# Kernel tuning notes

Measured on AMD Instinct MI355X. Metric: run time of the kernel, lower is better.

The kernel has to match this reference:

```python
import jax, jax.numpy as jnp
import numpy as np

HEADS = 12
WINDOW = 128

def setup_inputs() -> dict:
    key = jax.random.key(0)
    ks = jax.random.split(key, 5)
    B, N, C = 1, 4096, 768
    return {
        'x': jax.random.normal(ks[0], (B, N, C), dtype=jnp.float32),
        'qkv_w': jax.random.normal(ks[1], (3 * C, C), dtype=jnp.float32) * 0.02,
        'qkv_b': jax.random.normal(ks[2], (3 * C,), dtype=jnp.float32) * 0.02,
        'proj_w': jax.random.normal(ks[3], (C, C), dtype=jnp.float32) * 0.02,
        'proj_b': jax.random.normal(ks[4], (C,), dtype=jnp.float32) * 0.02,
    }

def reference(x, qkv_w, qkv_b, proj_w, proj_b):
    B, N, C = x.shape
    H = HEADS
    hd = C // H
    # qkv projection (torch Linear: y = x @ W^T + b)
    qkv = x @ qkv_w.T + qkv_b                      # [B, N, 3C]
    qkv = qkv.reshape(B, N, 3, H, hd).transpose(2, 0, 3, 1, 4)  # [3, B, H, N, hd]
    q, k, v = qkv[0], qkv[1], qkv[2]               # each [B, H, N, hd]
    # local (banded) mask: |i - j| <= window_size
    idxs = jnp.arange(N)
    local = jnp.abs(idxs[:, None] - idxs[None, :]) <= WINDOW  # [N, N] bool
    # dense scores then mask (faithful to original O(N^2) math)
    attn = jnp.einsum('bhnd,bhmd->bhnm', q, k) / jnp.sqrt(jnp.float32(hd))
    attn = jnp.where(local[None, None], attn, -jnp.inf)
    attn = jax.nn.softmax(attn, axis=-1)
    out = jnp.einsum('bhnm,bhmd->bhnd', attn, v)   # [B, H, N, hd]
    out = out.transpose(0, 2, 1, 3).reshape(B, N, C)
    return out @ proj_w.T + proj_b
```

## Files before the change

### kernel.cpp

```cpp
#include <hip/hip_runtime.h>
#include <hip/hip_fp16.h>
#include <cmath>

typedef _Float16 f16;
typedef __attribute__((ext_vector_type(8))) _Float16 f16x8;
typedef __attribute__((ext_vector_type(4))) _Float16 f16x4;
typedef __attribute__((ext_vector_type(4))) float f32x4;

#define EXP2F(x) __builtin_amdgcn_exp2f(x)


__global__ void pack3_f32_f16(
    const float* __restrict__ s0, f16* __restrict__ d0, int nc0, int kc0,
    const float* __restrict__ s1, f16* __restrict__ d1, int nc1, int kc1,
    const float* __restrict__ s2, f16* __restrict__ d2, int nc2, int kc2)
{
    int wid  = (blockIdx.x * blockDim.x + threadIdx.x) >> 6;
    int lane = threadIdx.x & 63;
    const float* s; f16* d; int cid, KC;
    if (wid < nc0)                  { s = s0; d = d0; cid = wid;             KC = kc0; }
    else if (wid < nc0 + nc1)       { s = s1; d = d1; cid = wid - nc0;       KC = kc1; }
    else if (wid < nc0 + nc1 + nc2) { s = s2; d = d2; cid = wid - nc0 - nc1; KC = kc2; }
    else return;
    int rc = cid / KC, kc = cid % KC;
    int K  = KC << 5;
    const float* src = s + (size_t)(rc * 16 + (lane & 15)) * K + kc * 32 + (lane >> 4) * 8;
    float4 v0 = *(const float4*)src;
    float4 v1 = *(const float4*)(src + 4);
    f16x8 o = { (f16)v0.x, (f16)v0.y, (f16)v0.z, (f16)v0.w,
                (f16)v1.x, (f16)v1.y, (f16)v1.z, (f16)v1.w };
    *(f16x8*)(d + (size_t)cid * 512 + lane * 8) = o;
}

__device__ __forceinline__ void store4(f16* p, const f32x4& v) {
    f16x4 o = { (f16)v[0], (f16)v[1], (f16)v[2], (f16)v[3] };
    *(f16x4*)p = o;
}
__device__ __forceinline__ void store4(float* p, const f32x4& v) {
    float4 o = { v[0], v[1], v[2], v[3] };
    *(float4*)p = o;
}

template <int WR, int WC, int MT, int NT, typename OT>
__global__ __launch_bounds__(256) void gemm_f16_packed(
    const f16* __restrict__ Ap,
    const f16* __restrict__ Wp,
    const float* __restrict__ bias,
    OT* __restrict__ out,
    int M, int N, int K)
{
    constexpr int KK  = 2;
    constexpr int ACH = WR * MT * KK;
    constexpr int BCH = WC * NT * KK;
    constexpr int AR  = ACH / 4;
    constexpr int BR  = BCH / 4;
    __shared__ f16 Ash[2][ACH * 512];
    __shared__ f16 Bsh[2][BCH * 512];

    const int tid  = threadIdx.x;
    const int lane = tid & 63;
    const int w    = tid >> 6;
    const int wr   = w / WC;
    const int wc   = w % WC;
    const int lr   = lane & 15;
    const int lq   = lane >> 4;
    const int bm   = blockIdx.y * (WR * MT * 16);
    const int bn   = blockIdx.x * (WC * NT * 16);
    const int KC   = K >> 5;

    const f16* ga[AR];
    const f16* gb[BR];
#pragma unroll
    for (int r = 0; r < AR; ++r) {
        int s = w * AR + r, rl = s / KK, kk = s % KK;
        ga[r] = Ap + ((size_t)((bm >> 4) + rl) * KC + kk) * 512 + lane * 8;
    }
#pragma unroll
    for (int r = 0; r < BR; ++r) {
        int s = w * BR + r, rl = s / KK, kk = s % KK;
        gb[r] = Wp + ((size_t)((bn >> 4) + rl) * KC + kk) * 512 + lane * 8;
    }

    f32x4 acc[MT][NT] = {};
    f16x8 sa[AR], sb[BR];

#pragma unroll
    for (int r = 0; r < AR; ++r) sa[r] = *(const f16x8*)(ga[r]);
#pragma unroll
    for (int r = 0; r < BR; ++r) sb[r] = *(const f16x8*)(gb[r]);
#pragma unroll
    for (int r = 0; r < AR; ++r) *(f16x8*)&Ash[0][(w * AR + r) * 512 + lane * 8] = sa[r];
#pragma unroll
    for (int r = 0; r < BR; ++r) *(f16x8*)&Bsh[0][(w * BR + r) * 512 + lane * 8] = sb[r];
    __syncthreads();

    const int nk = K >> 6;
    for (int k = 0; k < nk; ++k) {
        const int cur = k & 1;
        if (k + 1 < nk) {
            const int ko = (k + 1) * KK * 512;
#pragma unroll
            for (int r = 0; r < AR; ++r) sa[r] = *(const f16x8*)(ga[r] + ko);
#pragma unroll
            for (int r = 0; r < BR; ++r) sb[r] = *(const f16x8*)(gb[r] + ko);
        }
        f16x8 af[MT][KK], bf[NT][KK];
#pragma unroll
        for (int mt = 0; mt < MT; ++mt)
#pragma unroll
            for (int kk = 0; kk < KK; ++kk)
                af[mt][kk] = *(const f16x8*)&Ash[cur][((wr * MT + mt) * KK + kk) * 512 + lane * 8];
#pragma unroll
        for (int nt = 0; nt < NT; ++nt)
#pragma unroll
            for (int kk = 0; kk < KK; ++kk)
                bf[nt][kk] = *(const f16x8*)&Bsh[cur][((wc * NT + nt) * KK + kk) * 512 + lane * 8];
#pragma unroll
        for (int kk = 0; kk < KK; ++kk)
#pragma unroll
            for (int mt = 0; mt < MT; ++mt)
#pragma unroll
                for (int nt = 0; nt < NT; ++nt)
                    acc[mt][nt] = __builtin_amdgcn_mfma_f32_16x16x32_f16(
                        bf[nt][kk], af[mt][kk], acc[mt][nt], 0, 0, 0);
        if (k + 1 < nk) {
#pragma unroll
            for (int r = 0; r < AR; ++r)
                *(f16x8*)&Ash[cur ^ 1][(w * AR + r) * 512 + lane * 8] = sa[r];
#pragma unroll
            for (int r = 0; r < BR; ++r)
                *(f16x8*)&Bsh[cur ^ 1][(w * BR + r) * 512 + lane * 8] = sb[r];
        }
        __syncthreads();
    }

#pragma unroll
    for (int mt = 0; mt < MT; ++mt) {
        int row = bm + (wr * MT + mt) * 16 + lr;
#pragma unroll
        for (int nt = 0; nt < NT; ++nt) {
            int col = bn + (wc * NT + nt) * 16 + lq * 4;
            float4 bv = *(const float4*)(bias + col);
            f32x4 ov = acc[mt][nt];
            ov[0] += bv.x; ov[1] += bv.y; ov[2] += bv.z; ov[3] += bv.w;
            store4(out + (size_t)row * N + col, ov);
        }
    }
}

#define WINDOW_SZ 128

__global__ __launch_bounds__(256) void local_attn_mfma(
    const f16* __restrict__ qkv,
    f16* __restrict__ outp,
    int N)
{
    const int C  = 768;
    const int C3 = 2304;
    __shared__ f16 Ks[2][4096];
    __shared__ f16 Vt[2][4096];
    __shared__ f16 Ps[4096];

    const int tid  = threadIdx.x;
    const int lane = tid & 63;
    const int w    = tid >> 6;
    const int r15  = lane & 15;
    const int q4   = lane >> 4;
    const int ntiles = N >> 6;
    const int h  = blockIdx.x / ntiles;
    const int i0 = (blockIdx.x % ntiles) << 6;
    const int qoff = h * 64;
    const int koff = 768 + h * 64;
    const int voff = 1536 + h * 64;

    f16x8 qf[2];
    {
        const f16* qrow = qkv + (size_t)(i0 + w * 16 + r15) * C3 + qoff + q4 * 8;
        qf[0] = *(const f16x8*)(qrow);
        qf[1] = *(const f16x8*)(qrow + 32);
        const f16 qs = (f16)0.18033688f;
#pragma unroll
        for (int j = 0; j < 8; ++j) { qf[0][j] *= qs; qf[1][j] *= qs; }
    }

    const int vc0 = tid >> 3;
    const int vd0 = (tid & 7) * 8;
    const int va  = vd0 >> 3;

    f32x4 o[4] = {};
    float m_l = -1.0e30f, l_l = 0.f;

    const int lo = (i0 >= 128) ? 0 : ((128 - i0) >> 6);
    int hi = (N + 64 - i0) >> 6; if (hi > 4) hi = 4;

    f16x8 k0, k1, v0, v1;
    {
        int jbase = i0 - 128 + lo * 64;
        const f16* kr = qkv + (size_t)(jbase + w * 16 + r15) * C3 + koff + q4 * 8;
        k0 = *(const f16x8*)(kr);
        k1 = *(const f16x8*)(kr + 32);
        v0 = *(const f16x8*)(qkv + (size_t)(jbase + vc0) * C3 + voff + vd0);
        v1 = *(const f16x8*)(qkv + (size_t)(jbase + vc0 + 32) * C3 + voff + vd0);
        *(f16x8*)&Ks[0][(w * 2 + 0) * 512 + lane * 8] = k0;
        *(f16x8*)&Ks[0][(w * 2 + 1) * 512 + lane * 8] = k1;
        int cc0 = vc0 >> 3, c7 = vc0 & 7;
#pragma unroll
        for (int j = 0; j < 8; ++j) {
            Vt[0][(vd0 + j) * 64 + ((cc0 ^ va ^ j) & 7) * 8 + c7] = v0[j];
            Vt[0][(vd0 + j) * 64 + (((cc0 + 4) ^ va ^ j) & 7) * 8 + c7] = v1[j];
        }
    }
    __syncthreads();

    for (int ch = lo; ch <= hi; ++ch) {
        const int p = (ch - lo) & 1;
        const int jbase = i0 - 128 + ch * 64;
        const bool need_mask = (ch == 0) || (ch == 4);

        if (ch < hi) {
            int jn = jbase + 64;
            const f16* kr = qkv + (size_t)(jn + w * 16 + r15) * C3 + koff + q4 * 8;
            k0 = *(const f16x8*)(kr);
            k1 = *(const f16x8*)(kr + 32);
            v0 = *(const f16x8*)(qkv + (size_t)(jn + vc0) * C3 + voff + vd0);
            v1 = *(const f16x8*)(qkv + (size_t)(jn + vc0 + 32) * C3 + voff + vd0);
        }

        f32x4 s[4] = {};
#pragma unroll
        for (int ks = 0; ks < 2; ++ks)
#pragma unroll
            for (int nt = 0; nt < 4; ++nt) {
                f16x8 kf = *(const f16x8*)&Ks[p][(nt * 2 + ks) * 512 + lane * 8];
                s[nt] = __builtin_amdgcn_mfma_f32_16x16x32_f16(kf, qf[ks], s[nt], 0, 0, 0);
            }

        if (need_mask) {
            int qg = i0 + w * 16 + r15;
#pragma unroll
            for (int nt = 0; nt < 4; ++nt)
#pragma unroll
                for (int r = 0; r < 4; ++r) {
                    int dist = qg - (jbase + nt * 16 + q4 * 4 + r);
                    if (dist < 0) dist = -dist;
                    if (dist > WINDOW_SZ) s[nt][r] = -3.0e38f;
                }
        }

        float rmax = -3.0e38f;
#pragma unroll
        for (int nt = 0; nt < 4; ++nt)
#pragma unroll
            for (int r = 0; r < 4; ++r) rmax = fmaxf(rmax, s[nt][r]);
        rmax = fmaxf(rmax, __shfl_xor(rmax, 16));
        rmax = fmaxf(rmax, __shfl_xor(rmax, 32));
        float mn = fmaxf(m_l, rmax);
        float al = EXP2F(m_l - mn);
        m_l = mn;
        float rs = 0.f;
#pragma unroll
        for (int nt = 0; nt < 4; ++nt)
#pragma unroll
            for (int r = 0; r < 4; ++r) {
                float pv = EXP2F(s[nt][r] - mn);
                s[nt][r] = pv;
                rs += pv;
            }
        rs += __shfl_xor(rs, 16);
        rs += __shfl_xor(rs, 32);
        l_l = l_l * al + rs;
#pragma unroll
        for (int nd = 0; nd < 4; ++nd)
#pragma unroll
            for (int r = 0; r < 4; ++r) o[nd][r] *= al;

#pragma unroll
        for (int nt = 0; nt < 4; ++nt)
#pragma unroll
            for (int r = 0; r < 4; ++r) {
                int c  = nt * 16 + q4 * 4 + r;
                int cs = c >> 5;
                int c5 = c & 31;
                int ls = (c5 >> 3) * 16 + r15;
                int lss = ls ^ ((ls >> 3) & 7);
                Ps[(w * 2 + cs) * 512 + lss * 8 + (c5 & 7)] = (f16)s[nt][r];
            }

        int lssr = lane ^ ((lane >> 3) & 7);
#pragma unroll
        for (int cs = 0; cs < 2; ++cs) {
            f16x8 pf = *(const f16x8*)&Ps[(w * 2 + cs) * 512 + lssr * 8];
#pragma unroll
            for (int nd = 0; nd < 4; ++nd) {
                int d = nd * 16 + r15;
                int x = ((cs * 4 + q4) ^ (d >> 3) ^ d) & 7;
                f16x8 vf = *(const f16x8*)&Vt[p][d * 64 + x * 8];
                o[nd] = __builtin_amdgcn_mfma_f32_16x16x32_f16(vf, pf, o[nd], 0, 0, 0);
            }
        }

        if (ch < hi) {
            *(f16x8*)&Ks[p ^ 1][(w * 2 + 0) * 512 + lane * 8] = k0;
            *(f16x8*)&Ks[p ^ 1][(w * 2 + 1) * 512 + lane * 8] = k1;
            int cc0 = vc0 >> 3, c7 = vc0 & 7;
#pragma unroll
            for (int j = 0; j < 8; ++j) {
                Vt[p ^ 1][(vd0 + j) * 64 + ((cc0 ^ va ^ j) & 7) * 8 + c7] = v0[j];
                Vt[p ^ 1][(vd0 + j) * 64 + (((cc0 + 4) ^ va ^ j) & 7) * 8 + c7] = v1[j];
            }
        }
        __syncthreads();
    }

    float inv = 1.0f / l_l;
    const int KC2 = C >> 5;
    const int rc  = (i0 >> 4) + w;
#pragma unroll
    for (int nd = 0; nd < 4; ++nd) {
        int col = qoff + nd * 16 + q4 * 4;
        int kc  = col >> 5;
        int lp  = r15 + ((col >> 3) & 3) * 16;
        f16x4 ov = { (f16)(o[nd][0] * inv), (f16)(o[nd][1] * inv),
                     (f16)(o[nd][2] * inv), (f16)(o[nd][3] * inv) };
        *(f16x4*)(outp + ((size_t)rc * KC2 + kc) * 512 + lp * 8 + (col & 7)) = ov;
    }
}

extern "C" void kernel_launch(void* const* d_in, const int* in_sizes, int n_in,
                              void* d_out, int out_size, void* d_ws, size_t ws_size,
                              hipStream_t stream) {
    (void)n_in; (void)out_size; (void)ws_size;
    const float* x      = (const float*)d_in[0];
    const float* qkv_w  = (const float*)d_in[1];
    const float* qkv_b  = (const float*)d_in[2];
    const float* proj_w = (const float*)d_in[3];
    const float* proj_b = (const float*)d_in[4];
    float* outp = (float*)d_out;

    const int C    = in_sizes[2] / 3;
    const int Nseq = in_sizes[0] / C;
    const int C3   = 3 * C;
    const int KC   = C >> 5;

    char* ws = (char*)d_ws;
    f16* qkv_h = (f16*)ws;   ws += (size_t)Nseq * C3 * 2;
    f16* xp    = (f16*)ws;   ws += (size_t)Nseq * C * 2;
    f16* wqp   = (f16*)ws;   ws += (size_t)C3 * C * 2;
    f16* wpp   = (f16*)ws;
    f16* attn_p = xp;

    dim3 blk(256);
    {
        int nc0 = (Nseq / 16) * KC;
        int nc1 = (C3 / 16) * KC;
        int nc2 = (C / 16) * KC;
        int nwaves = nc0 + nc1 + nc2;
        pack3_f32_f16<<<dim3((nwaves + 3) / 4), blk, 0, stream>>>(
            x, xp, nc0, KC, qkv_w, wqp, nc1, KC, proj_w, wpp, nc2, KC);
    }
    gemm_f16_packed<2, 2, 4, 4, f16><<<dim3(C3 / 128, Nseq / 128), blk, 0, stream>>>(
        xp, wqp, qkv_b, qkv_h, Nseq, C3, C);
    local_attn_mfma<<<dim3((C / 64) * (Nseq / 64)), blk, 0, stream>>>(
        qkv_h, attn_p, Nseq);
    gemm_f16_packed<2, 2, 2, 2, float><<<dim3(C / 64, Nseq / 64), blk, 0, stream>>>(
        attn_p, wpp, proj_b, outp, Nseq, C, C);
}
```

Baseline: 133.3 us.

## Emit QKV in MFMA-fragment packed layout and read K/V directly from global

The QKV GEMM epilogue now writes Q and K per head in the MFMA operand fragment layout, and V transposed and packed, so the attention kernel can load operand fragments straight from global memory. The attention kernel drops its LDS double buffers for K and V, the register staging and the per-chunk __syncthreads, which removes LDS traffic and barrier stalls. In exchange, the GEMM epilogue does scattered scalar f16 stores for V. K/V reuse across the four waves of a block now depends on the cache rather than shared memory.

```diff
diff --git a/kernel.cpp b/kernel.cpp
--- a/kernel.cpp
+++ b/kernel.cpp
@@ -8,7 +8,6 @@
 typedef __attribute__((ext_vector_type(4))) float f32x4;
 
 #define EXP2F(x) __builtin_amdgcn_exp2f(x)
-
 
 __global__ void pack3_f32_f16(
     const float* __restrict__ s0, f16* __restrict__ d0, int nc0, int kc0,
@@ -41,7 +40,7 @@
     *(float4*)p = o;
 }
 
-template <int WR, int WC, int MT, int NT, typename OT>
+template <int WR, int WC, int MT, int NT, int MODE, typename OT>
 __global__ __launch_bounds__(256) void gemm_f16_packed(
     const f16* __restrict__ Ap,
     const f16* __restrict__ Wp,
@@ -143,7 +142,29 @@
             float4 bv = *(const float4*)(bias + col);
             f32x4 ov = acc[mt][nt];
             ov[0] += bv.x; ov[1] += bv.y; ov[2] += bv.z; ov[3] += bv.w;
-            store4(out + (size_t)row * N + col, ov);
+            if (MODE == 0) {
+                store4(out + (size_t)row * N + col, ov);
+            } else {
+                int tau = (col >= 1536) ? 2 : (col >= 768 ? 1 : 0);
+                int rm  = col - tau * 768;
+                int hh  = rm >> 6;
+                int d   = rm & 63;
+                f16* base = (f16*)out + ((size_t)tau * 12 + hh) * ((size_t)M * 64);
+                if (tau < 2) {
+                    size_t off = (size_t)(row >> 4) * 1024 + (d >> 5) * 512
+                               + (size_t)((row & 15) + ((d >> 3) & 3) * 16) * 8 + (d & 7);
+                    store4(base + off, ov);
+                } else {
+#pragma unroll
+                    for (int i = 0; i < 4; ++i) {
+                        int dd = d + i;
+                        size_t off = (size_t)(dd >> 4) * ((size_t)M * 16)
+                                   + (size_t)(row >> 5) * 512
+                                   + (size_t)((dd & 15) + ((row >> 3) & 3) * 16) * 8 + (row & 7);
+                        base[off] = (f16)ov[i];
+                    }
+                }
+            }
         }
     }
 }
@@ -151,14 +172,11 @@
 #define WINDOW_SZ 128
 
 __global__ __launch_bounds__(256) void local_attn_mfma(
-    const f16* __restrict__ qkv,
+    const f16* __restrict__ qkvp,
     f16* __restrict__ outp,
     int N)
 {
-    const int C  = 768;
-    const int C3 = 2304;
-    __shared__ f16 Ks[2][4096];
-    __shared__ f16 Vt[2][4096];
+    const int C = 768;
     __shared__ f16 Ps[4096];
 
     const int tid  = threadIdx.x;
@@ -169,23 +187,22 @@
     const int ntiles = N >> 6;
     const int h  = blockIdx.x / ntiles;
     const int i0 = (blockIdx.x % ntiles) << 6;
-    const int qoff = h * 64;
-    const int koff = 768 + h * 64;
-    const int voff = 1536 + h * 64;
+
+    const size_t hstride = (size_t)N * 64;
+    const f16* Qh = qkvp + (size_t)h * hstride;
+    const f16* Kh = qkvp + (size_t)(12 + h) * hstride;
+    const f16* Vh = qkvp + (size_t)(24 + h) * hstride;
+    const int dcStride = N * 16;
 
     f16x8 qf[2];
     {
-        const f16* qrow = qkv + (size_t)(i0 + w * 16 + r15) * C3 + qoff + q4 * 8;
-        qf[0] = *(const f16x8*)(qrow);
-        qf[1] = *(const f16x8*)(qrow + 32);
+        const f16* qp = Qh + (size_t)((i0 >> 4) + w) * 1024 + lane * 8;
+        qf[0] = *(const f16x8*)(qp);
+        qf[1] = *(const f16x8*)(qp + 512);
         const f16 qs = (f16)0.18033688f;
 #pragma unroll
         for (int j = 0; j < 8; ++j) { qf[0][j] *= qs; qf[1][j] *= qs; }
     }
-
-    const int vc0 = tid >> 3;
-    const int vd0 = (tid & 7) * 8;
-    const int va  = vd0 >> 3;
 
     f32x4 o[4] = {};
     float m_l = -1.0e30f, l_l = 0.f;
@@ -193,45 +210,19 @@
     const int lo = (i0 >= 128) ? 0 : ((128 - i0) >> 6);
     int hi = (N + 64 - i0) >> 6; if (hi > 4) hi = 4;
 
-    f16x8 k0, k1, v0, v1;
-    {
-        int jbase = i0 - 128 + lo * 64;
-        const f16* kr = qkv + (size_t)(jbase + w * 16 + r15) * C3 + koff + q4 * 8;
-        k0 = *(const f16x8*)(kr);
-        k1 = *(const f16x8*)(kr + 32);
-        v0 = *(const f16x8*)(qkv + (size_t)(jbase + vc0) * C3 + voff + vd0);
-        v1 = *(const f16x8*)(qkv + (size_t)(jbase + vc0 + 32) * C3 + voff + vd0);
-        *(f16x8*)&Ks[0][(w * 2 + 0) * 512 + lane * 8] = k0;
-        *(f16x8*)&Ks[0][(w * 2 + 1) * 512 + lane * 8] = k1;
-        int cc0 = vc0 >> 3, c7 = vc0 & 7;
-#pragma unroll
-        for (int j = 0; j < 8; ++j) {
-            Vt[0][(vd0 + j) * 64 + ((cc0 ^ va ^ j) & 7) * 8 + c7] = v0[j];
-            Vt[0][(vd0 + j) * 64 + (((cc0 + 4) ^ va ^ j) & 7) * 8 + c7] = v1[j];
-        }
-    }
-    __syncthreads();
+    const int lssr = lane ^ ((lane >> 3) & 7);
 
     for (int ch = lo; ch <= hi; ++ch) {
-        const int p = (ch - lo) & 1;
         const int jbase = i0 - 128 + ch * 64;
         const bool need_mask = (ch == 0) || (ch == 4);
 
-        if (ch < hi) {
-            int jn = jbase + 64;
-            const f16* kr = qkv + (size_t)(jn + w * 16 + r15) * C3 + koff + q4 * 8;
-            k0 = *(const f16x8*)(kr);
-            k1 = *(const f16x8*)(kr + 32);
-            v0 = *(const f16x8*)(qkv + (size_t)(jn + vc0) * C3 + voff + vd0);
-            v1 = *(const f16x8*)(qkv + (size_t)(jn + vc0 + 32) * C3 + voff + vd0);
-        }
-
         f32x4 s[4] = {};
 #pragma unroll
         for (int ks = 0; ks < 2; ++ks)
 #pragma unroll
             for (int nt = 0; nt < 4; ++nt) {
-                f16x8 kf = *(const f16x8*)&Ks[p][(nt * 2 + ks) * 512 + lane * 8];
+                f16x8 kf = *(const f16x8*)(Kh + (size_t)((jbase >> 4) + nt) * 1024
+                                              + ks * 512 + lane * 8);
                 s[nt] = __builtin_amdgcn_mfma_f32_16x16x32_f16(kf, qf[ks], s[nt], 0, 0, 0);
             }
 
@@ -286,30 +277,16 @@
                 Ps[(w * 2 + cs) * 512 + lss * 8 + (c5 & 7)] = (f16)s[nt][r];
             }
 
-        int lssr = lane ^ ((lane >> 3) & 7);
 #pragma unroll
         for (int cs = 0; cs < 2; ++cs) {
             f16x8 pf = *(const f16x8*)&Ps[(w * 2 + cs) * 512 + lssr * 8];
 #pragma unroll
             for (int nd = 0; nd < 4; ++nd) {
-                int d = nd * 16 + r15;
-                int x = ((cs * 4 + q4) ^ (d >> 3) ^ d) & 7;
-                f16x8 vf = *(const f16x8*)&Vt[p][d * 64 + x * 8];
+                f16x8 vf = *(const f16x8*)(Vh + (size_t)nd * dcStride
+                                              + (size_t)((jbase >> 5) + cs) * 512 + lane * 8);
                 o[nd] = __builtin_amdgcn_mfma_f32_16x16x32_f16(vf, pf, o[nd], 0, 0, 0);
             }
         }
-
-        if (ch < hi) {
-            *(f16x8*)&Ks[p ^ 1][(w * 2 + 0) * 512 + lane * 8] = k0;
-            *(f16x8*)&Ks[p ^ 1][(w * 2 + 1) * 512 + lane * 8] = k1;
-            int cc0 = vc0 >> 3, c7 = vc0 & 7;
-#pragma unroll
-            for (int j = 0; j < 8; ++j) {
-                Vt[p ^ 1][(vd0 + j) * 64 + ((cc0 ^ va ^ j) & 7) * 8 + c7] = v0[j];
-                Vt[p ^ 1][(vd0 + j) * 64 + (((cc0 + 4) ^ va ^ j) & 7) * 8 + c7] = v1[j];
-            }
-        }
-        __syncthreads();
     }
 
     float inv = 1.0f / l_l;
@@ -317,7 +294,7 @@
     const int rc  = (i0 >> 4) + w;
 #pragma unroll
     for (int nd = 0; nd < 4; ++nd) {
-        int col = qoff + nd * 16 + q4 * 4;
+        int col = h * 64 + nd * 16 + q4 * 4;
         int kc  = col >> 5;
         int lp  = r15 + ((col >> 3) & 3) * 16;
         f16x4 ov = { (f16)(o[nd][0] * inv), (f16)(o[nd][1] * inv),
@@ -343,7 +320,7 @@
     const int KC   = C >> 5;
 
     char* ws = (char*)d_ws;
-    f16* qkv_h = (f16*)ws;   ws += (size_t)Nseq * C3 * 2;
+    f16* qkv_p = (f16*)ws;   ws += (size_t)Nseq * C3 * 2;
     f16* xp    = (f16*)ws;   ws += (size_t)Nseq * C * 2;
     f16* wqp   = (f16*)ws;   ws += (size_t)C3 * C * 2;
     f16* wpp   = (f16*)ws;
@@ -358,10 +335,10 @@
         pack3_f32_f16<<<dim3((nwaves + 3) / 4), blk, 0, stream>>>(
             x, xp, nc0, KC, qkv_w, wqp, nc1, KC, proj_w, wpp, nc2, KC);
     }
-    gemm_f16_packed<2, 2, 4, 4, f16><<<dim3(C3 / 128, Nseq / 128), blk, 0, stream>>>(
-        xp, wqp, qkv_b, qkv_h, Nseq, C3, C);
+    gemm_f16_packed<2, 2, 4, 4, 1, f16><<<dim3(C3 / 128, Nseq / 128), blk, 0, stream>>>(
+        xp, wqp, qkv_b, qkv_p, Nseq, C3, C);
     local_attn_mfma<<<dim3((C / 64) * (Nseq / 64)), blk, 0, stream>>>(
-        qkv_h, attn_p, Nseq);
-    gemm_f16_packed<2, 2, 2, 2, float><<<dim3(C / 64, Nseq / 64), blk, 0, stream>>>(
+        qkv_p, attn_p, Nseq);
+    gemm_f16_packed<2, 2, 2, 2, 0, float><<<dim3(C / 64, Nseq / 64), blk, 0, stream>>>(
         attn_p, wpp, proj_b, outp, Nseq, C, C);
 }
```

New measurement: 130.6 us. 2.1% less time.
